# Kernel tuning notes

Measured on AMD Instinct MI355X. Metric: run time of the kernel, lower is better.

Reference implementation:

```python
import jax, jax.numpy as jnp
import numpy as np

B, S, E, H = 4, 1024, 512, 8
DK = E // H


def setup_inputs() -> dict:
    key = jax.random.key(0)
    ks = jax.random.split(key, 16)
    s = 1.0 / np.sqrt(E)
    inp = {
        "query": jax.random.normal(ks[0], (B, S, E), dtype=jnp.float32),
        "key": jax.random.normal(ks[1], (B, S, E), dtype=jnp.float32),
        "value": jax.random.normal(ks[2], (B, S, E), dtype=jnp.float32),
        "dist_conv": jax.random.uniform(ks[3], (B, S, S), dtype=jnp.float32),
        "mask": jax.random.randint(ks[4], (B, S, S), 0, 2, dtype=jnp.int32),
        # four Linear(E, E) layers: q, k, v, out (torch: y = x @ W.T + b)
        "Wq": jax.random.normal(ks[5], (E, E), dtype=jnp.float32) * s,
        "bq": jnp.zeros((E,), dtype=jnp.float32),
        "Wk": jax.random.normal(ks[6], (E, E), dtype=jnp.float32) * s,
        "bk": jnp.zeros((E,), dtype=jnp.float32),
        "Wv": jax.random.normal(ks[7], (E, E), dtype=jnp.float32) * s,
        "bv": jnp.zeros((E,), dtype=jnp.float32),
        "Wo": jax.random.normal(ks[8], (E, E), dtype=jnp.float32) * s,
        "bo": jnp.zeros((E,), dtype=jnp.float32),
        # 1x1 Conv2d(1, H) -> ReLU -> 1x1 Conv2d(H, H)
        "cw1": jax.random.normal(ks[9], (H,), dtype=jnp.float32),  # [out_c] (in_c=1, k=1)
        "cb1": jnp.zeros((H,), dtype=jnp.float32),
        "cw2": jax.random.normal(ks[10], (H, H), dtype=jnp.float32) * (1.0 / np.sqrt(H)),
        "cb2": jnp.zeros((H,), dtype=jnp.float32),
    }
    return inp


def reference(query, key, value, dist_conv, mask, Wq, bq, Wk, bk, Wv, bv, Wo, bo, cw1, cb1, cw2, cb2):
    # projections, split into heads: [B, H, S, DK]
    def proj(x, W, b):
        y = jnp.einsum("bse,fe->bsf", x, W) + b
        return y.reshape(B, S, H, DK).transpose(0, 2, 1, 3)

    q = proj(query, Wq, bq)
    k = proj(key, Wk, bk)
    v = proj(value, Wv, bv)

    # 1x1 conv stack on distance matrix: [B,S,S] -> [B,H,S,S]
    t = jax.nn.relu(dist_conv[:, None] * cw1[None, :, None, None] + cb1[None, :, None, None])
    bias = jnp.einsum("bhij,gh->bgij", t, cw2) + cb2[None, :, None, None]

    scores = jnp.einsum("bhqd,bhkd->bhqk", q, k) / jnp.sqrt(jnp.float32(DK))
    scores = scores * bias
    scores = jnp.where(mask[:, None] == 0, jnp.float32(-1e9), scores)
    p_attn = jax.nn.softmax(scores, axis=-1)

    x = jnp.einsum("bhqk,bhkd->bhqd", p_attn, v)
    x = x.transpose(0, 2, 1, 3).reshape(B, S, E)
    return jnp.einsum("bse,fe->bsf", x, Wo) + bo
```

## Files before the change

kernel.cpp:

```cpp
#include <hip/hip_runtime.h>
#include <hip/hip_bf16.h>
#include <math.h>

#define B_ 4
#define S_ 1024
#define E_ 512
#define H_ 8
#define DK_ 64

typedef short bf16x8 __attribute__((ext_vector_type(8)));
typedef float f32x4 __attribute__((ext_vector_type(4)));

#define MFMA16(a, b, c) __builtin_amdgcn_mfma_f32_16x16x32_bf16((a), (b), (c), 0, 0, 0)
#define cfence() asm volatile("" ::: "memory")

__device__ __forceinline__ void gl_lds16(const void* gptr, void* lptr) {
    __builtin_amdgcn_global_load_lds(
        (const __attribute__((address_space(1))) unsigned int*)gptr,
        (__attribute__((address_space(3))) unsigned int*)lptr,
        16, 0, 0);
}

__device__ __forceinline__ unsigned short bf16_bits(float v) {
    __hip_bfloat16 h = __float2bfloat16(v);
    return *(unsigned short*)&h;
}

__global__ __launch_bounds__(256) void prep(
    const float* __restrict__ q, const float* __restrict__ k, const float* __restrict__ v,
    const float* __restrict__ wq, const float* __restrict__ wk,
    const float* __restrict__ wv, const float* __restrict__ wo,
    const float* __restrict__ dist, const int* __restrict__ mask,
    const float* __restrict__ cw1, const float* __restrict__ cb1,
    const float* __restrict__ cw2, const float* __restrict__ cb2,
    __hip_bfloat16* qc, __hip_bfloat16* kc, __hip_bfloat16* vc,
    __hip_bfloat16* wqc, __hip_bfloat16* wkc, __hip_bfloat16* wvc, __hip_bfloat16* woc,
    __hip_bfloat16* __restrict__ biasS) {
    const int blk = blockIdx.x;
    if (blk >= 3584) {
        const int bi = blk - 3584;
        const int b = bi >> 10, i = bi & 1023;
        const int j0 = threadIdx.x * 4;
        const size_t dbase = ((size_t)b * 1024 + i) * 1024 + j0;
        float4 d4 = *(const float4*)(dist + dbase);
        int4 m4 = *(const int4*)(mask + dbase);
        float dv[4] = {d4.x, d4.y, d4.z, d4.w};
        int mv[4] = {m4.x, m4.y, m4.z, m4.w};
        float tt[4][8];
#pragma unroll
        for (int e = 0; e < 4; ++e)
#pragma unroll
            for (int h = 0; h < 8; ++h)
                tt[e][h] = fmaxf(fmaf(dv[e], cw1[h], cb1[h]), 0.f);
#pragma unroll
        for (int g = 0; g < 8; ++g) {
            const float c2 = cb2[g];
            union { unsigned short us[4]; uint2 u2; } o;
#pragma unroll
            for (int e = 0; e < 4; ++e) {
                float bv = c2;
#pragma unroll
                for (int h = 0; h < 8; ++h) bv = fmaf(tt[e][h], cw2[g * 8 + h], bv);
                unsigned short u = bf16_bits(bv * 0.125f);
                if (mv[e] == 0) u = 0xFF80u;
                o.us[e] = u;
            }
            *(uint2*)(biasS + ((size_t)(b * 8 + g) * 1024 + i) * 1024 + j0) = o.u2;
        }
        return;
    }
    const float* src;
    __hip_bfloat16* dst;
    int base;
    if (blk < 1024)      { src = q; dst = qc; base = blk; }
    else if (blk < 2048) { src = k; dst = kc; base = blk - 1024; }
    else if (blk < 3072) { src = v; dst = vc; base = blk - 2048; }
    else {
        const int wz = (blk - 3072) >> 7;
        base = (blk - 3072) & 127;
        switch (wz) {
            case 0: src = wq; dst = wqc; break;
            case 1: src = wk; dst = wkc; break;
            case 2: src = wv; dst = wvc; break;
            default: src = wo; dst = woc; break;
        }
    }
    const int idx = (base * 256 + threadIdx.x) * 8;
    float4 a = *(const float4*)(src + idx);
    float4 bb = *(const float4*)(src + idx + 4);
    union { __hip_bfloat16 h[8]; uint4 u; } o;
    o.h[0] = __float2bfloat16(a.x);  o.h[1] = __float2bfloat16(a.y);
    o.h[2] = __float2bfloat16(a.z);  o.h[3] = __float2bfloat16(a.w);
    o.h[4] = __float2bfloat16(bb.x); o.h[5] = __float2bfloat16(bb.y);
    o.h[6] = __float2bfloat16(bb.z); o.h[7] = __float2bfloat16(bb.w);
    *(uint4*)(dst + idx) = o.u;
}

template <int NROWS_W, int NT>
__device__ __forceinline__ void gemm_core128(const __hip_bfloat16* A, const __hip_bfloat16* W,
                                             char* sA, char* sW, int m0, int n0,
                                             f32x4 acc[4][NT]) {
    const int t = threadIdx.x;
    const int w = t >> 6, lane = t & 63;
    const int wm = (w >> 1) * 64, wn = (w & 1) * (NT * 16);
    const int g = lane >> 4, ln = lane & 15;

    for (int kc = 0; kc < 4; ++kc) {
        __syncthreads();
#pragma unroll
        for (int i = 0; i < 8; ++i) {
            int L = (i * 4 + w) * 64 + lane;
            int r = L >> 4, cs = L & 15;
            int c = cs ^ (r & 15);
            gl_lds16((const char*)A + (size_t)(m0 + r) * 1024 + kc * 256 + c * 16,
                     sA + (i * 4 + w) * 1024);
        }
#pragma unroll
        for (int i = 0; i < NROWS_W / 16; ++i) {
            int L = (i * 4 + w) * 64 + lane;
            int r = L >> 4, cs = L & 15;
            int c = cs ^ (r & 15);
            gl_lds16((const char*)W + (size_t)(n0 + r) * 1024 + kc * 256 + c * 16,
                     sW + (i * 4 + w) * 1024);
        }
        __syncthreads();
#pragma unroll
        for (int ks = 0; ks < 4; ++ks) {
            bf16x8 af[4], bf[NT];
#pragma unroll
            for (int mt = 0; mt < 4; ++mt) {
                int m = wm + mt * 16 + ln;
                int c = ks * 4 + g;
                af[mt] = *(const bf16x8*)(sA + m * 256 + (c ^ (m & 15)) * 16);
            }
#pragma unroll
            for (int nt = 0; nt < NT; ++nt) {
                int n = wn + nt * 16 + ln;
                int c = ks * 4 + g;
                bf[nt] = *(const bf16x8*)(sW + n * 256 + (c ^ (n & 15)) * 16);
            }
#pragma unroll
            for (int mt = 0; mt < 4; ++mt)
#pragma unroll
                for (int nt = 0; nt < NT; ++nt)
                    acc[mt][nt] = MFMA16(af[mt], bf[nt], acc[mt][nt]);
        }
    }
}

__global__ __launch_bounds__(256) void proj_gemm(
    const __hip_bfloat16* __restrict__ qc, const __hip_bfloat16* __restrict__ kc,
    const __hip_bfloat16* __restrict__ vc,
    const __hip_bfloat16* __restrict__ wqc, const __hip_bfloat16* __restrict__ wkc,
    const __hip_bfloat16* __restrict__ wvc,
    const float* __restrict__ bq, const float* __restrict__ bk, const float* __restrict__ bv,
    __hip_bfloat16* qbh, __hip_bfloat16* kbh, __hip_bfloat16* vt) {
    __shared__ char smem[65536];
    char* sA = smem;
    char* sW = smem + 32768;
    const int z = blockIdx.z;
    const __hip_bfloat16* A;
    const __hip_bfloat16* W;
    const float* bias;
    __hip_bfloat16* dst;
    if (z == 0)      { A = qc; W = wqc; bias = bq; dst = qbh; }
    else if (z == 1) { A = kc; W = wkc; bias = bk; dst = kbh; }
    else             { A = vc; W = wvc; bias = bv; dst = vt; }

    const int m0 = blockIdx.y * 128, n0 = blockIdx.x * 128;
    f32x4 acc[4][4] = {};
    gemm_core128<128, 4>(A, W, sA, sW, m0, n0, acc);
    __syncthreads();

    const int t = threadIdx.x;
    const int w = t >> 6, lane = t & 63;
    const int wm = (w >> 1) * 64, wn = (w & 1) * 64;
    const int g = lane >> 4, ln = lane & 15;
    const int b = m0 >> 10;
    float bv4[4];
#pragma unroll
    for (int nt = 0; nt < 4; ++nt) bv4[nt] = bias[n0 + wn + nt * 16 + ln];

    __hip_bfloat16* T = (__hip_bfloat16*)smem;
    if (z != 2) {
#pragma unroll
        for (int p = 0; p < 2; ++p) {
            if (wm == p * 64) {
#pragma unroll
                for (int mt = 0; mt < 4; ++mt)
#pragma unroll
                    for (int nt = 0; nt < 4; ++nt)
#pragma unroll
                        for (int r = 0; r < 4; ++r)
                            T[(mt * 16 + g * 4 + r) * 136 + wn + nt * 16 + ln] =
                                __float2bfloat16(acc[mt][nt][r] + bv4[nt]);
            }
            __syncthreads();
            const int lr = t >> 2, quarter = t & 3;
            const char* srow = (const char*)T + lr * 272 + quarter * 64;
            const int s = (m0 & 1023) + p * 64 + lr;
            const int h = (n0 >> 6) + (quarter >> 1);
            char* gdst = (char*)dst +
                         (((size_t)(b * 8 + h) * 1024 + s) * 64 + (quarter & 1) * 32) * 2;
#pragma unroll
            for (int j = 0; j < 4; ++j)
                *(uint4*)(gdst + j * 16) = *(const uint4*)(srow + j * 16);
            __syncthreads();
        }
    } else {
#pragma unroll
        for (int p = 0; p < 2; ++p) {
            if (wm == p * 64) {
#pragma unroll
                for (int mt = 0; mt < 4; ++mt)
#pragma unroll
                    for (int nt = 0; nt < 4; ++nt)
#pragma unroll
                        for (int r = 0; r < 4; ++r)
                            T[(mt * 16 + g * 4 + r) * 130 + wn + nt * 16 + ln] =
                                __float2bfloat16(acc[mt][nt][r] + bv4[nt]);
            }
            __syncthreads();
            const int c = t >> 1, sel = t & 1;
            union { __hip_bfloat16 h[32]; uint4 u[4]; } P;
#pragma unroll
            for (int i = 0; i < 32; ++i)
                P.h[i] = T[(sel * 32 + i) * 130 + c];
            const int h = (n0 >> 6) + (c >> 6), dk = c & 63;
            char* gdst = (char*)vt +
                         (((size_t)(b * 8 + h) * 64 + dk) * 1024 + (m0 & 1023) + p * 64 + sel * 32) * 2;
#pragma unroll
            for (int j = 0; j < 4; ++j)
                *(uint4*)(gdst + j * 16) = P.u[j];
            __syncthreads();
        }
    }
}

__global__ __launch_bounds__(256) void out_gemm(
    const __hip_bfloat16* __restrict__ X, const __hip_bfloat16* __restrict__ woc,
    const float* __restrict__ bo, float* __restrict__ out) {
    __shared__ char smem[49152];
    char* sA = smem;
    char* sW = smem + 32768;
    const int m0 = blockIdx.y * 128, n0 = blockIdx.x * 64;
    f32x4 acc[4][2] = {};
    gemm_core128<64, 2>(X, woc, sA, sW, m0, n0, acc);

    const int t = threadIdx.x;
    const int w = t >> 6, lane = t & 63;
    const int wm = (w >> 1) * 64, wn = (w & 1) * 32;
    const int g = lane >> 4, ln = lane & 15;
    float bv2[2];
#pragma unroll
    for (int nt = 0; nt < 2; ++nt) bv2[nt] = bo[n0 + wn + nt * 16 + ln];
#pragma unroll
    for (int mt = 0; mt < 4; ++mt)
#pragma unroll
        for (int nt = 0; nt < 2; ++nt)
#pragma unroll
            for (int r = 0; r < 4; ++r) {
                int m = m0 + wm + mt * 16 + g * 4 + r;
                int f = n0 + wn + nt * 16 + ln;
                out[(size_t)m * 512 + f] = acc[mt][nt][r] + bv2[nt];
            }
}

__global__ __launch_bounds__(256) void attn(
    const __hip_bfloat16* __restrict__ Qb, const __hip_bfloat16* __restrict__ Kb,
    const __hip_bfloat16* __restrict__ Vt, const __hip_bfloat16* __restrict__ biasS,
    __hip_bfloat16* __restrict__ X) {
    __shared__ char sK[16384];
    __shared__ char sV[16384];
    __shared__ char sScP[4][4352];
    __shared__ float sBr[4][16];

    const int t = threadIdx.x, w = t >> 6, lane = t & 63;
    const int g = lane >> 4, ln = lane & 15;
    const int qr = lane >> 2, a = lane & 3;
    const int bh = blockIdx.y;
    const int q0 = blockIdx.x * 64;

    float* sc = (float*)(sScP[w]);
    __hip_bfloat16* sp = (__hip_bfloat16*)(sScP[w]);

    bf16x8 qf[2];
    {
        const char* qbase = (const char*)Qb + ((size_t)bh * 1024 + q0 + w * 16 + ln) * 128;
        qf[0] = *(const bf16x8*)(qbase + g * 16);
        qf[1] = *(const bf16x8*)(qbase + 64 + g * 16);
    }

    float m_st = -1e30f, l_st = 0.f;
    f32x4 O[4] = {};

    const size_t kbase = (size_t)bh * 1024 * 128;
    const size_t vbase = (size_t)bh * 64 * 2048;
    const __hip_bfloat16* brow = biasS + ((size_t)bh * 1024 + q0 + w * 16 + qr) * 1024;

    for (int kt = 0; kt < S_; kt += 128) {
        __syncthreads();
#pragma unroll
        for (int i = 0; i < 4; ++i) {
            int L = (i * 4 + w) * 64 + lane;
            int r = L >> 3, cs = L & 7;
            int c = cs ^ (r & 7);
            gl_lds16((const char*)Kb + kbase + (size_t)(kt + r) * 128 + c * 16,
                     sK + (i * 4 + w) * 1024);
        }
#pragma unroll
        for (int i = 0; i < 4; ++i) {
            int L = (i * 4 + w) * 64 + lane;
            int r = L >> 4, cs = L & 15;
            int c = cs ^ (r & 15);
            gl_lds16((const char*)Vt + vbase + (size_t)r * 2048 + (size_t)kt * 2 + c * 16,
                     sV + (i * 4 + w) * 1024);
        }
        union { uint4 u[2]; unsigned short us[16]; } bb[2];
#pragma unroll
        for (int ph = 0; ph < 2; ++ph) {
            bb[ph].u[0] = *(const uint4*)(brow + kt + ph * 64 + a * 16);
            bb[ph].u[1] = *(const uint4*)(brow + kt + ph * 64 + a * 16 + 8);
        }
        __syncthreads();

#pragma unroll
        for (int ph = 0; ph < 2; ++ph) {
            f32x4 scv[4] = {};
#pragma unroll
            for (int tt = 0; tt < 4; ++tt)
#pragma unroll
                for (int ks = 0; ks < 2; ++ks) {
                    int key = ph * 64 + tt * 16 + ln;
                    int c = ks * 4 + g;
                    bf16x8 kf = *(const bf16x8*)(sK + key * 128 + (c ^ (key & 7)) * 16);
                    scv[tt] = MFMA16(qf[ks], kf, scv[tt]);
                }

            cfence();
#pragma unroll
            for (int tt = 0; tt < 4; ++tt)
#pragma unroll
                for (int r = 0; r < 4; ++r)
                    sc[(g * 4 + r) * 66 + tt * 16 + ln] = scv[tt][r];
            cfence();

            float sr[16];
            {
                const float* scrow = sc + qr * 66 + a * 16;
#pragma unroll
                for (int j = 0; j < 8; ++j) {
                    float2 v2 = *(const float2*)(scrow + j * 2);
                    sr[j * 2] = v2.x; sr[j * 2 + 1] = v2.y;
                }
            }
            cfence();

            float mx = -1e30f;
#pragma unroll
            for (int e = 0; e < 16; ++e) {
                unsigned int bits = bb[ph].us[e];
                float f = __uint_as_float(bits << 16);
                float s = sr[e] * f;
                s = (bits == 0xFF80u) ? -1e9f : s;
                sr[e] = s;
                mx = fmaxf(mx, s);
            }
            mx = fmaxf(mx, __shfl_xor(mx, 1));
            mx = fmaxf(mx, __shfl_xor(mx, 2));
            const float mnew = fmaxf(m_st, mx);
            const float alpha = __expf(m_st - mnew);
            m_st = mnew;
            float rs = 0.f;
            union { __hip_bfloat16 hh16[16]; uint4 u[2]; } Pk;
#pragma unroll
            for (int i = 0; i < 16; ++i) {
                float p = __expf(sr[i] - mnew);
                rs += p;
                Pk.hh16[i] = __float2bfloat16(p);
            }
            rs += __shfl_xor(rs, 1);
            rs += __shfl_xor(rs, 2);
            l_st = l_st * alpha + rs;

            *(uint4*)(sp + qr * 72 + a * 16) = Pk.u[0];
            *(uint4*)(sp + qr * 72 + a * 16 + 8) = Pk.u[1];
            cfence();

            if (a == 0) sBr[w][qr] = alpha;
            float al4[4];
#pragma unroll
            for (int r = 0; r < 4; ++r) al4[r] = sBr[w][g * 4 + r];
#pragma unroll
            for (int tt = 0; tt < 4; ++tt)
#pragma unroll
                for (int r = 0; r < 4; ++r) O[tt][r] *= al4[r];

#pragma unroll
            for (int ks = 0; ks < 2; ++ks) {
                bf16x8 pf = *(const bf16x8*)(sp + ln * 72 + ks * 32 + g * 8);
#pragma unroll
                for (int tt = 0; tt < 4; ++tt) {
                    int dk = tt * 16 + ln;
                    int ck = ph * 8 + ks * 4 + g;
                    bf16x8 vf = *(const bf16x8*)(sV + dk * 256 + (ck ^ (dk & 15)) * 16);
                    O[tt] = MFMA16(pf, vf, O[tt]);
                }
            }
            cfence();
        }
    }

    if (a == 0) sBr[w][qr] = l_st;
    __builtin_amdgcn_s_waitcnt(0);
    const int b = bh >> 3, h = bh & 7;
#pragma unroll
    for (int r = 0; r < 4; ++r) {
        float inv = 1.f / sBr[w][g * 4 + r];
        int q = q0 + w * 16 + g * 4 + r;
#pragma unroll
        for (int tt = 0; tt < 4; ++tt) {
            int dk = tt * 16 + ln;
            X[((size_t)(b * 1024 + q)) * 512 + h * 64 + dk] = __float2bfloat16(O[tt][r] * inv);
        }
    }
}

extern "C" void kernel_launch(void* const* d_in, const int* in_sizes, int n_in,
                              void* d_out, int out_size, void* d_ws, size_t ws_size,
                              hipStream_t stream) {
    (void)in_sizes; (void)n_in; (void)out_size; (void)ws_size;
    const float* query = (const float*)d_in[0];
    const float* key   = (const float*)d_in[1];
    const float* value = (const float*)d_in[2];
    const float* dist  = (const float*)d_in[3];
    const int*   mask  = (const int*)d_in[4];
    const float* Wq = (const float*)d_in[5];
    const float* bq = (const float*)d_in[6];
    const float* Wk = (const float*)d_in[7];
    const float* bk = (const float*)d_in[8];
    const float* Wv = (const float*)d_in[9];
    const float* bv = (const float*)d_in[10];
    const float* Wo = (const float*)d_in[11];
    const float* bo = (const float*)d_in[12];
    const float* cw1 = (const float*)d_in[13];
    const float* cb1 = (const float*)d_in[14];
    const float* cw2 = (const float*)d_in[15];
    const float* cb2 = (const float*)d_in[16];
    float* out = (float*)d_out;

    char* ws = (char*)d_ws;
    const size_t MB = 1 << 20;
    __hip_bfloat16* qc  = (__hip_bfloat16*)(ws + 0 * MB);
    __hip_bfloat16* kc  = (__hip_bfloat16*)(ws + 4 * MB);
    __hip_bfloat16* vc  = (__hip_bfloat16*)(ws + 8 * MB);
    __hip_bfloat16* wqc = (__hip_bfloat16*)(ws + 12 * MB);
    __hip_bfloat16* wkc = (__hip_bfloat16*)(ws + 12 * MB + 512 * 1024);
    __hip_bfloat16* wvc = (__hip_bfloat16*)(ws + 13 * MB);
    __hip_bfloat16* woc = (__hip_bfloat16*)(ws + 13 * MB + 512 * 1024);
    __hip_bfloat16* qbh = (__hip_bfloat16*)(ws + 14 * MB);
    __hip_bfloat16* kbh = (__hip_bfloat16*)(ws + 18 * MB);
    __hip_bfloat16* vt  = (__hip_bfloat16*)(ws + 22 * MB);
    __hip_bfloat16* x   = (__hip_bfloat16*)(ws + 26 * MB);
    __hip_bfloat16* bS  = (__hip_bfloat16*)(ws + 32 * MB);

    hipLaunchKernelGGL(prep, dim3(7680), dim3(256), 0, stream,
                       query, key, value, Wq, Wk, Wv, Wo, dist, mask,
                       cw1, cb1, cw2, cb2,
                       qc, kc, vc, wqc, wkc, wvc, woc, bS);
    hipLaunchKernelGGL(proj_gemm, dim3(4, 32, 3), dim3(256), 0, stream,
                       qc, kc, vc, wqc, wkc, wvc, bq, bk, bv, qbh, kbh, vt);
    hipLaunchKernelGGL(attn, dim3(16, 32), dim3(256), 0, stream,
                       qbh, kbh, vt, bS, x);
    hipLaunchKernelGGL(out_gemm, dim3(8, 32), dim3(256), 0, stream,
                       x, woc, bo, out);
}
```

Measured before the change: 197.8 us.

## Split attention over key range in two halves and combine partial softmax results

```diff
diff --git a/kernel.cpp b/kernel.cpp
--- a/kernel.cpp
+++ b/kernel.cpp
@@ -266,12 +266,12 @@
             }
 }
 
-__global__ __launch_bounds__(256) void attn(
+__global__ __launch_bounds__(256) void attn_split(
     const __hip_bfloat16* __restrict__ Qb, const __hip_bfloat16* __restrict__ Kb,
     const __hip_bfloat16* __restrict__ Vt, const __hip_bfloat16* __restrict__ biasS,
-    __hip_bfloat16* __restrict__ X) {
-    __shared__ char sK[16384];
-    __shared__ char sV[16384];
+    float* __restrict__ Op, float2* __restrict__ Ml) {
+    __shared__ char sK[8192];
+    __shared__ char sV[8192];
     __shared__ char sScP[4][4352];
     __shared__ float sBr[4][16];
 
@@ -280,6 +280,8 @@
     const int qr = lane >> 2, a = lane & 3;
     const int bh = blockIdx.y;
     const int q0 = blockIdx.x * 64;
+    const int spl = blockIdx.z;
+    const int kt0 = spl * 512;
 
     float* sc = (float*)(sScP[w]);
     __hip_bfloat16* sp = (__hip_bfloat16*)(sScP[w]);
@@ -291,139 +293,154 @@
         qf[1] = *(const bf16x8*)(qbase + 64 + g * 16);
     }
 
+    const char* kaddr[2];
+    const char* vaddr[2];
+#pragma unroll
+    for (int i = 0; i < 2; ++i) {
+        int L = (i * 4 + w) * 64 + lane;
+        int r = L >> 3, cs = L & 7;
+        int c = cs ^ (r & 7);
+        kaddr[i] = (const char*)Kb + (size_t)bh * 131072 + (size_t)(kt0 + r) * 128 + c * 16;
+        vaddr[i] = (const char*)Vt + (size_t)bh * 131072 + (size_t)r * 2048 + (size_t)kt0 * 2 + c * 16;
+    }
+    const char* baddr =
+        (const char*)(biasS + ((size_t)bh * 1024 + q0 + w * 16 + qr) * 1024 + kt0 + a * 16);
+
     float m_st = -1e30f, l_st = 0.f;
     f32x4 O[4] = {};
 
-    const size_t kbase = (size_t)bh * 1024 * 128;
-    const size_t vbase = (size_t)bh * 64 * 2048;
-    const __hip_bfloat16* brow = biasS + ((size_t)bh * 1024 + q0 + w * 16 + qr) * 1024;
-
-    for (int kt = 0; kt < S_; kt += 128) {
+    for (int it = 0; it < 8; ++it) {
         __syncthreads();
 #pragma unroll
-        for (int i = 0; i < 4; ++i) {
-            int L = (i * 4 + w) * 64 + lane;
-            int r = L >> 3, cs = L & 7;
-            int c = cs ^ (r & 7);
-            gl_lds16((const char*)Kb + kbase + (size_t)(kt + r) * 128 + c * 16,
-                     sK + (i * 4 + w) * 1024);
-        }
-#pragma unroll
-        for (int i = 0; i < 4; ++i) {
-            int L = (i * 4 + w) * 64 + lane;
-            int r = L >> 4, cs = L & 15;
-            int c = cs ^ (r & 15);
-            gl_lds16((const char*)Vt + vbase + (size_t)r * 2048 + (size_t)kt * 2 + c * 16,
-                     sV + (i * 4 + w) * 1024);
-        }
-        union { uint4 u[2]; unsigned short us[16]; } bb[2];
-#pragma unroll
-        for (int ph = 0; ph < 2; ++ph) {
-            bb[ph].u[0] = *(const uint4*)(brow + kt + ph * 64 + a * 16);
-            bb[ph].u[1] = *(const uint4*)(brow + kt + ph * 64 + a * 16 + 8);
-        }
+        for (int i = 0; i < 2; ++i) {
+            gl_lds16(kaddr[i], sK + (i * 4 + w) * 1024);
+            gl_lds16(vaddr[i], sV + (i * 4 + w) * 1024);
+            kaddr[i] += 8192;
+            vaddr[i] += 128;
+        }
+        union { uint4 u[2]; unsigned short us[16]; } bb;
+        bb.u[0] = *(const uint4*)baddr;
+        bb.u[1] = *(const uint4*)(baddr + 16);
+        baddr += 128;
         __syncthreads();
 
-#pragma unroll
-        for (int ph = 0; ph < 2; ++ph) {
-            f32x4 scv[4] = {};
-#pragma unroll
-            for (int tt = 0; tt < 4; ++tt)
-#pragma unroll
-                for (int ks = 0; ks < 2; ++ks) {
-                    int key = ph * 64 + tt * 16 + ln;
-                    int c = ks * 4 + g;
-                    bf16x8 kf = *(const bf16x8*)(sK + key * 128 + (c ^ (key & 7)) * 16);
-                    scv[tt] = MFMA16(qf[ks], kf, scv[tt]);
-                }
-
-            cfence();
-#pragma unroll
-            for (int tt = 0; tt < 4; ++tt)
-#pragma unroll
-                for (int r = 0; r < 4; ++r)
-                    sc[(g * 4 + r) * 66 + tt * 16 + ln] = scv[tt][r];
-            cfence();
-
-            float sr[16];
-            {
-                const float* scrow = sc + qr * 66 + a * 16;
-#pragma unroll
-                for (int j = 0; j < 8; ++j) {
-                    float2 v2 = *(const float2*)(scrow + j * 2);
-                    sr[j * 2] = v2.x; sr[j * 2 + 1] = v2.y;
-                }
-            }
-            cfence();
-
-            float mx = -1e30f;
-#pragma unroll
-            for (int e = 0; e < 16; ++e) {
-                unsigned int bits = bb[ph].us[e];
-                float f = __uint_as_float(bits << 16);
-                float s = sr[e] * f;
-                s = (bits == 0xFF80u) ? -1e9f : s;
-                sr[e] = s;
-                mx = fmaxf(mx, s);
-            }
-            mx = fmaxf(mx, __shfl_xor(mx, 1));
-            mx = fmaxf(mx, __shfl_xor(mx, 2));
-            const float mnew = fmaxf(m_st, mx);
-            const float alpha = __expf(m_st - mnew);
-            m_st = mnew;
-            float rs = 0.f;
-            union { __hip_bfloat16 hh16[16]; uint4 u[2]; } Pk;
-#pragma unroll
-            for (int i = 0; i < 16; ++i) {
-                float p = __expf(sr[i] - mnew);
-                rs += p;
-                Pk.hh16[i] = __float2bfloat16(p);
-            }
-            rs += __shfl_xor(rs, 1);
-            rs += __shfl_xor(rs, 2);
-            l_st = l_st * alpha + rs;
-
-            *(uint4*)(sp + qr * 72 + a * 16) = Pk.u[0];
-            *(uint4*)(sp + qr * 72 + a * 16 + 8) = Pk.u[1];
-            cfence();
-
-            if (a == 0) sBr[w][qr] = alpha;
-            float al4[4];
-#pragma unroll
-            for (int r = 0; r < 4; ++r) al4[r] = sBr[w][g * 4 + r];
-#pragma unroll
-            for (int tt = 0; tt < 4; ++tt)
-#pragma unroll
-                for (int r = 0; r < 4; ++r) O[tt][r] *= al4[r];
-
+        f32x4 scv[4] = {};
+#pragma unroll
+        for (int tt = 0; tt < 4; ++tt)
 #pragma unroll
             for (int ks = 0; ks < 2; ++ks) {
-                bf16x8 pf = *(const bf16x8*)(sp + ln * 72 + ks * 32 + g * 8);
-#pragma unroll
-                for (int tt = 0; tt < 4; ++tt) {
-                    int dk = tt * 16 + ln;
-                    int ck = ph * 8 + ks * 4 + g;
-                    bf16x8 vf = *(const bf16x8*)(sV + dk * 256 + (ck ^ (dk & 15)) * 16);
-                    O[tt] = MFMA16(pf, vf, O[tt]);
-                }
-            }
-            cfence();
-        }
-    }
-
-    if (a == 0) sBr[w][qr] = l_st;
-    __builtin_amdgcn_s_waitcnt(0);
-    const int b = bh >> 3, h = bh & 7;
+                int key = tt * 16 + ln;
+                int c = ks * 4 + g;
+                bf16x8 kf = *(const bf16x8*)(sK + key * 128 + (c ^ (key & 7)) * 16);
+                scv[tt] = MFMA16(qf[ks], kf, scv[tt]);
+            }
+
+        cfence();
+#pragma unroll
+        for (int tt = 0; tt < 4; ++tt)
+#pragma unroll
+            for (int r = 0; r < 4; ++r)
+                sc[(g * 4 + r) * 66 + tt * 16 + ln] = scv[tt][r];
+        cfence();
+
+        float sr[16];
+        {
+            const float* scrow = sc + qr * 66 + a * 16;
+#pragma unroll
+            for (int j = 0; j < 8; ++j) {
+                float2 v2 = *(const float2*)(scrow + j * 2);
+                sr[j * 2] = v2.x; sr[j * 2 + 1] = v2.y;
+            }
+        }
+        cfence();
+
+        float mx = -1e30f;
+#pragma unroll
+        for (int e = 0; e < 16; ++e) {
+            unsigned int bits = bb.us[e];
+            float f = __uint_as_float(bits << 16);
+            float s = sr[e] * f;
+            s = (bits == 0xFF80u) ? -1e9f : s;
+            sr[e] = s;
+            mx = fmaxf(mx, s);
+        }
+        mx = fmaxf(mx, __shfl_xor(mx, 1));
+        mx = fmaxf(mx, __shfl_xor(mx, 2));
+        const float mnew = fmaxf(m_st, mx);
+        const float alpha = __expf(m_st - mnew);
+        m_st = mnew;
+        float rs = 0.f;
+        union { __hip_bfloat16 hh16[16]; uint4 u[2]; } Pk;
+#pragma unroll
+        for (int i = 0; i < 16; ++i) {
+            float p = __expf(sr[i] - mnew);
+            rs += p;
+            Pk.hh16[i] = __float2bfloat16(p);
+        }
+        rs += __shfl_xor(rs, 1);
+        rs += __shfl_xor(rs, 2);
+        l_st = l_st * alpha + rs;
+
+        *(uint4*)(sp + qr * 72 + a * 16) = Pk.u[0];
+        *(uint4*)(sp + qr * 72 + a * 16 + 8) = Pk.u[1];
+        cfence();
+
+        if (a == 0) sBr[w][qr] = alpha;
+        float al4[4];
+#pragma unroll
+        for (int r = 0; r < 4; ++r) al4[r] = sBr[w][g * 4 + r];
+#pragma unroll
+        for (int tt = 0; tt < 4; ++tt)
+#pragma unroll
+            for (int r = 0; r < 4; ++r) O[tt][r] *= al4[r];
+
+#pragma unroll
+        for (int ks = 0; ks < 2; ++ks) {
+            bf16x8 pf = *(const bf16x8*)(sp + ln * 72 + ks * 32 + g * 8);
+#pragma unroll
+            for (int tt = 0; tt < 4; ++tt) {
+                int dk = tt * 16 + ln;
+                int c = ks * 4 + g;
+                bf16x8 vf = *(const bf16x8*)(sV + dk * 128 + (c ^ (dk & 7)) * 16);
+                O[tt] = MFMA16(pf, vf, O[tt]);
+            }
+        }
+        cfence();
+    }
+
+    const size_t rowbase = ((size_t)spl * 32 + bh) * 1024 + q0 + w * 16;
+    if (a == 0) {
+        float2 ml2; ml2.x = m_st; ml2.y = l_st;
+        Ml[rowbase + qr] = ml2;
+    }
 #pragma unroll
     for (int r = 0; r < 4; ++r) {
-        float inv = 1.f / sBr[w][g * 4 + r];
-        int q = q0 + w * 16 + g * 4 + r;
-#pragma unroll
-        for (int tt = 0; tt < 4; ++tt) {
-            int dk = tt * 16 + ln;
-            X[((size_t)(b * 1024 + q)) * 512 + h * 64 + dk] = __float2bfloat16(O[tt][r] * inv);
-        }
-    }
+        const int q = g * 4 + r;
+#pragma unroll
+        for (int tt = 0; tt < 4; ++tt)
+            Op[(rowbase + q) * 64 + tt * 16 + ln] = O[tt][r];
+    }
+}
+
+__global__ __launch_bounds__(256) void combine(
+    const float* __restrict__ Op, const float2* __restrict__ Ml,
+    __hip_bfloat16* __restrict__ X) {
+    const int idx = blockIdx.x * 256 + threadIdx.x;
+    const int row = idx >> 5;
+    const int pr = (idx & 31) * 2;
+    float2 ml1 = Ml[row], ml2 = Ml[32768 + row];
+    float m = fmaxf(ml1.x, ml2.x);
+    float w1 = __expf(ml1.x - m), w2 = __expf(ml2.x - m);
+    float inv = 1.f / fmaf(ml1.y, w1, ml2.y * w2);
+    float2 o1 = *(const float2*)(Op + (size_t)row * 64 + pr);
+    float2 o2 = *(const float2*)(Op + ((size_t)32768 + row) * 64 + pr);
+    float x0 = fmaf(o1.x, w1, o2.x * w2) * inv;
+    float x1 = fmaf(o1.y, w1, o2.y * w2) * inv;
+    const int bh = row >> 10, s = row & 1023, b = bh >> 3, h = bh & 7;
+    union { __hip_bfloat16 hh[2]; unsigned int u; } o;
+    o.hh[0] = __float2bfloat16(x0);
+    o.hh[1] = __float2bfloat16(x1);
+    *(unsigned int*)(X + ((size_t)(b * 1024 + s)) * 512 + h * 64 + pr) = o.u;
 }
 
 extern "C" void kernel_launch(void* const* d_in, const int* in_sizes, int n_in,
@@ -463,6 +480,8 @@
     __hip_bfloat16* vt  = (__hip_bfloat16*)(ws + 22 * MB);
     __hip_bfloat16* x   = (__hip_bfloat16*)(ws + 26 * MB);
     __hip_bfloat16* bS  = (__hip_bfloat16*)(ws + 32 * MB);
+    float*          Op  = (float*)(ws + 96 * MB);
+    float2*         Ml  = (float2*)(ws + 112 * MB);
 
     hipLaunchKernelGGL(prep, dim3(7680), dim3(256), 0, stream,
                        query, key, value, Wq, Wk, Wv, Wo, dist, mask,
@@ -470,8 +489,9 @@
                        qc, kc, vc, wqc, wkc, wvc, woc, bS);
     hipLaunchKernelGGL(proj_gemm, dim3(4, 32, 3), dim3(256), 0, stream,
                        qc, kc, vc, wqc, wkc, wvc, bq, bk, bv, qbh, kbh, vt);
-    hipLaunchKernelGGL(attn, dim3(16, 32), dim3(256), 0, stream,
-                       qbh, kbh, vt, bS, x);
+    hipLaunchKernelGGL(attn_split, dim3(16, 32, 2), dim3(256), 0, stream,
+                       qbh, kbh, vt, bS, Op, Ml);
+    hipLaunchKernelGGL(combine, dim3(4096), dim3(256), 0, stream, Op, Ml, x);
     hipLaunchKernelGGL(out_gemm, dim3(8, 32), dim3(256), 0, stream,
                        x, woc, bo, out);
 }
```

Result: no change. 196.1 us (-0.9%).
